# Kernel tuning notes

Hardware: AMD Instinct MI355X
Metric: run time of the kernel (lower is better)

## Reference

```python
import jax, jax.numpy as jnp
import numpy as np

N, S, R, M, C, CZ = 1, 128, 256, 256, 32, 128


def setup_inputs() -> dict:
    key = jax.random.key(0)
    k1, k2, k3, k4 = jax.random.split(key, 4)
    return {
        "msa_repr": jax.random.normal(k1, (N, S, R, M), dtype=jnp.float32) * 0.1,
        "left_w": jax.random.normal(k2, (M, C), dtype=jnp.float32) * 0.02,
        "right_w": jax.random.normal(k3, (M, C), dtype=jnp.float32) * 0.02,
        "out_w": jax.random.normal(k4, (C * C, CZ), dtype=jnp.float32) * 0.02,
    }


def reference(msa_repr, left_w, right_w, out_w):
    # msa_repr: [N,S,R,M]
    n, s, r, m = msa_repr.shape
    c = left_w.shape[1]
    # opm_projection: [N,S,R,M] @ [M,C] -> [N,S,R,C]
    left = jnp.einsum('nsrm,mc->nsrc', msa_repr, left_w)
    right = jnp.einsum('nsrm,mc->nsrc', msa_repr, right_w)
    # outer product summed over MSA dim s: [N,R,T,C,C]
    # (torch: a=left.transpose(-2,-3) -> [N,R,S,C]; einsum '...bac,...dae->...bdce')
    outer = jnp.einsum('nsrc,nste->nrtce', left, right).reshape(n, r, r, c * c)
    # project to pair channel: [N,R,T,C*C] @ [C*C,CZ] -> [N,R,T,CZ]
    return jnp.matmul(outer, out_w)
```

## Files before the change

kernel.cpp:

```cpp
#include <hip/hip_runtime.h>
#include <stdint.h>

#define S_DIM 128
#define R_DIM 256
#define M_DIM 256
#define C_DIM 32
#define CZ_DIM 128
#define K2_DIM 1024

typedef _Float16 f16;
typedef _Float16 f16x4 __attribute__((ext_vector_type(4)));
typedef _Float16 f16x8 __attribute__((ext_vector_type(8)));
typedef float f32x4 __attribute__((ext_vector_type(4)));
typedef float f32x16 __attribute__((ext_vector_type(16)));

__global__ void prep_kernel(const float* __restrict__ lw, const float* __restrict__ rw,
                            const float* __restrict__ ow,
                            f16* __restrict__ wt_l, f16* __restrict__ wt_r,
                            f16* __restrict__ wt2) {
    int idx = blockIdx.x * blockDim.x + threadIdx.x;
    int stride = gridDim.x * blockDim.x;
    for (int i = idx; i < CZ_DIM * K2_DIM; i += stride) {
        int cz = i >> 10, k2 = i & 1023;
        int c = k2 >> 5, e = k2 & 31;
        int k2p = ((e >> 2) << 7) + (c << 2) + (e & 3);
        int ntile = cz >> 5, l31 = cz & 31;
        int kk = k2p >> 4, q5 = (k2p >> 3) & 1, j = k2p & 7;
        wt2[(ntile * 64 + kk) * 512 + (l31 * 2 + q5) * 8 + j] = (f16)ow[k2 * CZ_DIM + cz];
    }
    for (int i = idx; i < C_DIM * M_DIM; i += stride) {
        int c = i >> 8, m = i & 255;
        wt_l[i] = (f16)lw[m * C_DIM + c];
        wt_r[i] = (f16)rw[m * C_DIM + c];
    }
}

__global__ __launch_bounds__(256, 4)
void proj_kernel(const float* __restrict__ msa, const f16* __restrict__ wt_l,
                 const f16* __restrict__ wt_r,
                 f16* __restrict__ left_t, f16* __restrict__ rt2) {
    int bid = blockIdx.x;
    int r  = bid >> 1;
    int s0 = (bid & 1) << 6;
    int tid = threadIdx.x;
    int w = tid >> 6;
    int lane = tid & 63;
    int q = lane >> 4, li = lane & 15;

    int s_col = s0 + w * 16 + li;
    const f32x4* bp = (const f32x4*)(msa + ((size_t)s_col * R_DIM + r) * M_DIM + q * 8);

    f32x4 b[16];
#pragma unroll
    for (int ks = 0; ks < 8; ks++) { b[2 * ks] = bp[ks * 8]; b[2 * ks + 1] = bp[ks * 8 + 1]; }

    f32x4 aL0 = {0,0,0,0}, aL1 = {0,0,0,0}, aR0 = {0,0,0,0}, aR1 = {0,0,0,0};
#pragma unroll
    for (int ks = 0; ks < 8; ks++) {
        f16x8 bf;
#pragma unroll
        for (int u = 0; u < 4; u++) { bf[u] = (f16)b[2*ks][u]; bf[4 + u] = (f16)b[2*ks+1][u]; }
        const f16* a0 = wt_l + li * M_DIM + ks * 32 + q * 8;
        const f16* a1 = wt_r + li * M_DIM + ks * 32 + q * 8;
        f16x8 al0 = *(const f16x8*)(a0);
        f16x8 al1 = *(const f16x8*)(a0 + 16 * M_DIM);
        f16x8 ar0 = *(const f16x8*)(a1);
        f16x8 ar1 = *(const f16x8*)(a1 + 16 * M_DIM);
        aL0 = __builtin_amdgcn_mfma_f32_16x16x32_f16(al0, bf, aL0, 0, 0, 0);
        aL1 = __builtin_amdgcn_mfma_f32_16x16x32_f16(al1, bf, aL1, 0, 0, 0);
        aR0 = __builtin_amdgcn_mfma_f32_16x16x32_f16(ar0, bf, aR0, 0, 0, 0);
        aR1 = __builtin_amdgcn_mfma_f32_16x16x32_f16(ar1, bf, aR1, 0, 0, 0);
    }
    int ks_s = s_col >> 4, q5_s = (s_col >> 3) & 1, j_s = s_col & 7;
    int sbase = (r * 8 + ks_s) * 512 + q5_s * 8 + j_s;
#pragma unroll
    for (int reg = 0; reg < 4; reg++) {
        int c0 = q * 4 + reg;
        left_t[(r * C_DIM + c0) * S_DIM + s_col]      = (f16)aL0[reg];
        left_t[(r * C_DIM + c0 + 16) * S_DIM + s_col] = (f16)aL1[reg];
        rt2[sbase + c0 * 16]        = (f16)aR0[reg];
        rt2[sbase + (c0 + 16) * 16] = (f16)aR1[reg];
    }
}

__global__ __launch_bounds__(512, 4)
void fuse_kernel(const f16* __restrict__ left_t, const f16* __restrict__ rt2,
                 const f16* __restrict__ wt2, float* __restrict__ out) {
    __shared__ __align__(16) char lds[65536];
    f16* Ls = (f16*)lds;

    int bid = blockIdx.x;
    int br = bid >> 6, bt = bid & 63;
    int tid = threadIdx.x;
    int w = tid >> 6, lane = tid & 63;
    int q5 = lane >> 5, l31 = lane & 31, lx = lane & 15;

    const f16* Lg = left_t + (size_t)br * 32768;

    int t_tile = w & 3, rg4 = w >> 2;
    int g = bt * 4 + t_tile;
    const f16* ap = rt2 + (size_t)g * 4096 + (l31 * 2 + q5) * 8;
    f16x8 afr[8];
#pragma unroll
    for (int ks = 0; ks < 8; ks++) afr[ks] = *(const f16x8*)(ap + ks * 512);

#pragma unroll
    for (int it = 0; it < 8; it++) {
        int G = it * 512 + tid, row = G >> 4, ch = G & 15;
        f16x8 v = *(const f16x8*)(Lg + G * 8);
        *(f16x8*)(Ls + row * 128 + ((ch ^ (row & 15)) << 3)) = v;
    }
    __syncthreads();

    f32x16 acc[4] = {};
#pragma unroll
    for (int i = 0; i < 4; i++) {
        const f16* bbase = Ls + ((rg4 * 4 + i) * 32 + l31) * 128;
#pragma unroll
        for (int ks = 0; ks < 8; ks++) {
            f16x8 bfr = *(const f16x8*)(bbase + (((2 * ks + q5) ^ lx) << 3));
            acc[i] = __builtin_amdgcn_mfma_f32_32x32x16_f16(afr[ks], bfr, acc[i], 0, 0, 0);
        }
    }

    int ntile = w & 3, kh = w >> 2;
    const f16* wbase = wt2 + (size_t)(ntile * 64 + kh * 32) * 512 + (l31 * 2 + q5) * 8;
    f16x8 wfg[8][4];
#pragma unroll
    for (int u = 0; u < 4; u++) wfg[0][u] = *(const f16x8*)(wbase + u * 512);

    __syncthreads();

    int chc = l31 >> 1, bsub = 8 * (l31 & 1);
#pragma unroll
    for (int i = 0; i < 4; i++) {
        int p = (rg4 * 4 + i) * 4 + t_tile;
        char* prow = lds + p * 2048;
#pragma unroll
        for (int rg = 0; rg < 4; rg++) {
            int ch = (2 * rg + q5) * 16 + chc;
            int phys = (ch + p) & 127;
            f16x4 h = {(f16)acc[i][4 * rg], (f16)acc[i][4 * rg + 1],
                       (f16)acc[i][4 * rg + 2], (f16)acc[i][4 * rg + 3]};
            *(f16x4*)(prow + phys * 16 + bsub) = h;
        }
    }
    __syncthreads();

    const char* lbase = lds + l31 * 2048;
    int base = 64 * kh + q5 + l31;
    f16x8 afg[8][4];
    f32x16 accA = {}, accB = {};
#pragma unroll
    for (int gg = 0; gg < 8; gg++) {
        if (gg == 0) {
#pragma unroll
            for (int u = 0; u < 4; u++) wfg[1][u] = *(const f16x8*)(wbase + (4 + u) * 512);
#pragma unroll
            for (int u = 0; u < 4; u++) wfg[2][u] = *(const f16x8*)(wbase + (8 + u) * 512);
#pragma unroll
            for (int u = 0; u < 4; u++)
                afg[0][u] = *(const f16x8*)(lbase + (((base + 2 * u) & 127) << 4));
#pragma unroll
            for (int u = 0; u < 4; u++)
                afg[1][u] = *(const f16x8*)(lbase + (((base + 8 + 2 * u) & 127) << 4));
        } else {
            if (gg + 2 < 8) {
#pragma unroll
                for (int u = 0; u < 4; u++)
                    wfg[gg + 2][u] = *(const f16x8*)(wbase + ((gg + 2) * 4 + u) * 512);
            }
            if (gg + 1 < 8) {
#pragma unroll
                for (int u = 0; u < 4; u++)
                    afg[gg + 1][u] = *(const f16x8*)(lbase + (((base + (gg + 1) * 8 + 2 * u) & 127) << 4));
            }
        }
        accA = __builtin_amdgcn_mfma_f32_32x32x16_f16(afg[gg][0], wfg[gg][0], accA, 0, 0, 0);
        accB = __builtin_amdgcn_mfma_f32_32x32x16_f16(afg[gg][1], wfg[gg][1], accB, 0, 0, 0);
        accA = __builtin_amdgcn_mfma_f32_32x32x16_f16(afg[gg][2], wfg[gg][2], accA, 0, 0, 0);
        accB = __builtin_amdgcn_mfma_f32_32x32x16_f16(afg[gg][3], wfg[gg][3], accB, 0, 0, 0);
    }
    f32x16 acc2;
#pragma unroll
    for (int v = 0; v < 16; v++) acc2[v] = accA[v] + accB[v];
    __syncthreads();

    if (w >= 4) {
        char* rb = lds + (w - 4) * 4096 + lane * 64;
#pragma unroll
        for (int u = 0; u < 4; u++) {
            f32x4 part = {acc2[4 * u], acc2[4 * u + 1], acc2[4 * u + 2], acc2[4 * u + 3]};
            *(f32x4*)(rb + u * 16) = part;
        }
    }
    __syncthreads();
    if (w < 4) {
        const char* rb = lds + w * 4096 + lane * 64;
#pragma unroll
        for (int u = 0; u < 4; u++) {
            f32x4 part = *(const f32x4*)(rb + u * 16);
#pragma unroll
            for (int v = 0; v < 4; v++) acc2[4 * u + v] += part[v];
        }
        int r0 = br * 8, t0 = bt * 4, cz = w * 32 + l31;
#pragma unroll
        for (int reg = 0; reg < 16; reg++) {
            int p = (reg & 3) + 8 * (reg >> 2) + 4 * q5;
            out[((size_t)((r0 + (p >> 2)) * R_DIM + t0 + (p & 3))) * CZ_DIM + cz] = acc2[reg];
        }
    }
}

extern "C" void kernel_launch(void* const* d_in, const int* in_sizes, int n_in,
                              void* d_out, int out_size, void* d_ws, size_t ws_size,
                              hipStream_t stream) {
    const float* msa = (const float*)d_in[0];
    const float* lw  = (const float*)d_in[1];
    const float* rw  = (const float*)d_in[2];
    const float* ow  = (const float*)d_in[3];
    char* ws = (char*)d_ws;
    f16* left_t = (f16*)(ws);
    f16* rt2    = (f16*)(ws + (size_t)2 * 1024 * 1024);
    f16* wt2    = (f16*)(ws + (size_t)4 * 1024 * 1024);
    f16* wt_l   = (f16*)(ws + (size_t)4 * 1024 * 1024 + 262144);
    f16* wt_r   = (f16*)(ws + (size_t)4 * 1024 * 1024 + 262144 + 16384);
    float* out  = (float*)d_out;

    prep_kernel<<<dim3(256), dim3(256), 0, stream>>>(lw, rw, ow, wt_l, wt_r, wt2);
    proj_kernel<<<dim3(512), dim3(256), 0, stream>>>(msa, wt_l, wt_r, left_t, rt2);
    fuse_kernel<<<dim3(2048), dim3(512), 0, stream>>>(left_t, rt2, wt2, out);
}
```

Before: 137.9 us.

## Fuse weight prep into projection kernel and pre-swizzle left tile for direct LDS load

Removes the separate prep kernel: each projection block converts the left/right projection weights into LDS itself and handles one slice of the output-weight reorder. The projection now writes the left operand already in the XOR-swizzled tile layout, so the fuse kernel can copy it straight into LDS with global_load_lds instead of staging through registers. This saves one launch and the register round trip, at the cost of every projection block redundantly converting 16K weight elements.

```diff
diff --git a/kernel.cpp b/kernel.cpp
--- a/kernel.cpp
+++ b/kernel.cpp
@@ -14,45 +14,51 @@
 typedef float f32x4 __attribute__((ext_vector_type(4)));
 typedef float f32x16 __attribute__((ext_vector_type(16)));
 
-__global__ void prep_kernel(const float* __restrict__ lw, const float* __restrict__ rw,
-                            const float* __restrict__ ow,
-                            f16* __restrict__ wt_l, f16* __restrict__ wt_r,
-                            f16* __restrict__ wt2) {
-    int idx = blockIdx.x * blockDim.x + threadIdx.x;
-    int stride = gridDim.x * blockDim.x;
-    for (int i = idx; i < CZ_DIM * K2_DIM; i += stride) {
-        int cz = i >> 10, k2 = i & 1023;
-        int c = k2 >> 5, e = k2 & 31;
-        int k2p = ((e >> 2) << 7) + (c << 2) + (e & 3);
-        int ntile = cz >> 5, l31 = cz & 31;
-        int kk = k2p >> 4, q5 = (k2p >> 3) & 1, j = k2p & 7;
-        wt2[(ntile * 64 + kk) * 512 + (l31 * 2 + q5) * 8 + j] = (f16)ow[k2 * CZ_DIM + cz];
-    }
-    for (int i = idx; i < C_DIM * M_DIM; i += stride) {
-        int c = i >> 8, m = i & 255;
-        wt_l[i] = (f16)lw[m * C_DIM + c];
-        wt_r[i] = (f16)rw[m * C_DIM + c];
-    }
-}
+typedef const __attribute__((address_space(1))) uint32_t gu32_t;
+typedef __attribute__((address_space(3))) uint32_t lu32_t;
+#define GLOAD_LDS16(g, l) \
+    __builtin_amdgcn_global_load_lds((gu32_t*)(g), (lu32_t*)(l), 16, 0, 0)
 
 __global__ __launch_bounds__(256, 4)
-void proj_kernel(const float* __restrict__ msa, const f16* __restrict__ wt_l,
-                 const f16* __restrict__ wt_r,
-                 f16* __restrict__ left_t, f16* __restrict__ rt2) {
+void proj_kernel(const float* __restrict__ msa, const float* __restrict__ lw,
+                 const float* __restrict__ rw, const float* __restrict__ ow,
+                 f16* __restrict__ left_t, f16* __restrict__ rt2,
+                 f16* __restrict__ wt2) {
+    __shared__ __align__(16) f16 wlT[8192];
+    __shared__ __align__(16) f16 wrT[8192];
+
     int bid = blockIdx.x;
-    int r  = bid >> 1;
-    int s0 = (bid & 1) << 6;
     int tid = threadIdx.x;
     int w = tid >> 6;
     int lane = tid & 63;
     int q = lane >> 4, li = lane & 15;
-
+    int r  = bid >> 1;
+    int s0 = (bid & 1) << 6;
     int s_col = s0 + w * 16 + li;
+
     const f32x4* bp = (const f32x4*)(msa + ((size_t)s_col * R_DIM + r) * M_DIM + q * 8);
-
     f32x4 b[16];
 #pragma unroll
     for (int ks = 0; ks < 8; ks++) { b[2 * ks] = bp[ks * 8]; b[2 * ks + 1] = bp[ks * 8 + 1]; }
+
+    {
+        int i = bid * 256 + tid;
+        int cz = i >> 10, k2 = i & 1023;
+        int c = k2 >> 5, e = k2 & 31;
+        int k2p = ((e >> 2) << 7) + (c << 2) + (e & 3);
+        int ntile = cz >> 5, l31o = cz & 31;
+        int kk = k2p >> 4, q5o = (k2p >> 3) & 1, j = k2p & 7;
+        wt2[(ntile * 64 + kk) * 512 + (l31o * 2 + q5o) * 8 + j] = (f16)ow[k2 * CZ_DIM + cz];
+    }
+#pragma unroll
+    for (int k = 0; k < 32; k++) {
+        int i = k * 256 + tid;
+        int m = i >> 5, c = i & 31;
+        int d = ((m >> 3) * 32 + c) * 8 + (m & 7);
+        wlT[d] = (f16)lw[i];
+        wrT[d] = (f16)rw[i];
+    }
+    __syncthreads();
 
     f32x4 aL0 = {0,0,0,0}, aL1 = {0,0,0,0}, aR0 = {0,0,0,0}, aR1 = {0,0,0,0};
 #pragma unroll
@@ -60,12 +66,12 @@
         f16x8 bf;
 #pragma unroll
         for (int u = 0; u < 4; u++) { bf[u] = (f16)b[2*ks][u]; bf[4 + u] = (f16)b[2*ks+1][u]; }
-        const f16* a0 = wt_l + li * M_DIM + ks * 32 + q * 8;
-        const f16* a1 = wt_r + li * M_DIM + ks * 32 + q * 8;
+        const f16* a0 = wlT + ((ks * 4 + q) * 32 + li) * 8;
+        const f16* a1 = wrT + ((ks * 4 + q) * 32 + li) * 8;
         f16x8 al0 = *(const f16x8*)(a0);
-        f16x8 al1 = *(const f16x8*)(a0 + 16 * M_DIM);
+        f16x8 al1 = *(const f16x8*)(a0 + 128);
         f16x8 ar0 = *(const f16x8*)(a1);
-        f16x8 ar1 = *(const f16x8*)(a1 + 16 * M_DIM);
+        f16x8 ar1 = *(const f16x8*)(a1 + 128);
         aL0 = __builtin_amdgcn_mfma_f32_16x16x32_f16(al0, bf, aL0, 0, 0, 0);
         aL1 = __builtin_amdgcn_mfma_f32_16x16x32_f16(al1, bf, aL1, 0, 0, 0);
         aR0 = __builtin_amdgcn_mfma_f32_16x16x32_f16(ar0, bf, aR0, 0, 0, 0);
@@ -73,11 +79,16 @@
     }
     int ks_s = s_col >> 4, q5_s = (s_col >> 3) & 1, j_s = s_col & 7;
     int sbase = (r * 8 + ks_s) * 512 + q5_s * 8 + j_s;
+    int rl = r & 7;
+    f16* Lb = left_t + (size_t)(r >> 3) * 32768;
+    int sc = s_col >> 3, sj = s_col & 7;
 #pragma unroll
     for (int reg = 0; reg < 4; reg++) {
         int c0 = q * 4 + reg;
-        left_t[(r * C_DIM + c0) * S_DIM + s_col]      = (f16)aL0[reg];
-        left_t[(r * C_DIM + c0 + 16) * S_DIM + s_col] = (f16)aL1[reg];
+        int row0 = rl * 32 + c0;
+        int swz = sc ^ c0;
+        Lb[(row0 * 16 + swz) * 8 + sj]        = (f16)aL0[reg];
+        Lb[((row0 + 16) * 16 + swz) * 8 + sj] = (f16)aL1[reg];
         rt2[sbase + c0 * 16]        = (f16)aR0[reg];
         rt2[sbase + (c0 + 16) * 16] = (f16)aR1[reg];
     }
@@ -97,6 +108,11 @@
 
     const f16* Lg = left_t + (size_t)br * 32768;
 
+#pragma unroll
+    for (int it = 0; it < 8; it++) {
+        GLOAD_LDS16(Lg + (size_t)(it * 512 + tid) * 8, Ls + (it * 512 + tid) * 8);
+    }
+
     int t_tile = w & 3, rg4 = w >> 2;
     int g = bt * 4 + t_tile;
     const f16* ap = rt2 + (size_t)g * 4096 + (l31 * 2 + q5) * 8;
@@ -104,12 +120,6 @@
 #pragma unroll
     for (int ks = 0; ks < 8; ks++) afr[ks] = *(const f16x8*)(ap + ks * 512);
 
-#pragma unroll
-    for (int it = 0; it < 8; it++) {
-        int G = it * 512 + tid, row = G >> 4, ch = G & 15;
-        f16x8 v = *(const f16x8*)(Lg + G * 8);
-        *(f16x8*)(Ls + row * 128 + ((ch ^ (row & 15)) << 3)) = v;
-    }
     __syncthreads();
 
     f32x16 acc[4] = {};
@@ -223,11 +233,8 @@
     f16* left_t = (f16*)(ws);
     f16* rt2    = (f16*)(ws + (size_t)2 * 1024 * 1024);
     f16* wt2    = (f16*)(ws + (size_t)4 * 1024 * 1024);
-    f16* wt_l   = (f16*)(ws + (size_t)4 * 1024 * 1024 + 262144);
-    f16* wt_r   = (f16*)(ws + (size_t)4 * 1024 * 1024 + 262144 + 16384);
     float* out  = (float*)d_out;
 
-    prep_kernel<<<dim3(256), dim3(256), 0, stream>>>(lw, rw, ow, wt_l, wt_r, wt2);
-    proj_kernel<<<dim3(512), dim3(256), 0, stream>>>(msa, wt_l, wt_r, left_t, rt2);
+    proj_kernel<<<dim3(512), dim3(256), 0, stream>>>(msa, lw, rw, ow, left_t, rt2, wt2);
     fuse_kernel<<<dim3(2048), dim3(512), 0, stream>>>(left_t, rt2, wt2, out);
 }
```

Result: faster. 131.7 us (-4.5%).
